# Performance work log

Measured on AMD Instinct MI355X. Metric: run time of the kernel, lower is better.

The kernel has to match this reference:

```python
import jax, jax.numpy as jnp
import numpy as np
from jax.ops import segment_sum, segment_max

N_NODES, SEQ, D, V = 2048, 64, 256, 32000
NH, DH = 8, 32      # transformer heads, head dim
GH = 4              # GAT heads (concat=False -> mean over heads)
E = 32768
NEG_INF = -1e9


def _pe(max_len, d):
    pos = np.arange(max_len)[:, None].astype(np.float32)
    div = np.exp(np.arange(0, d, 2).astype(np.float32) * (-np.log(10000.0) / d))
    pe = np.zeros((max_len, d), np.float32)
    pe[:, 0::2] = np.sin(pos * div)
    pe[:, 1::2] = np.cos(pos * div)
    return jnp.asarray(pe)


def _ln(x, g, b, eps=1e-5):
    m = x.mean(-1, keepdims=True)
    v = jnp.var(x, axis=-1, keepdims=True)
    return (x - m) / jnp.sqrt(v + eps) * g + b


def _encoder(x, Wqkv, bqkv, Wo, bo, ln1g, ln1b, ln2g, ln2b, W1, b1, W2, b2):
    # nn.TransformerEncoder, post-norm, relu, dropout off (eval)
    for l in range(2):
        qkv = x @ Wqkv[l] + bqkv[l]
        q, k, v = jnp.split(qkv, 3, -1)
        hds = lambda t: t.reshape(N_NODES, SEQ, NH, DH).transpose(0, 2, 1, 3)
        q, k, v = hds(q), hds(k), hds(v)
        att = jax.nn.softmax(jnp.einsum('bhqd,bhkd->bhqk', q, k) / np.sqrt(DH).astype(np.float32), -1)
        o = jnp.einsum('bhqk,bhkd->bhqd', att, v).transpose(0, 2, 1, 3).reshape(N_NODES, SEQ, D)
        x = _ln(x + o @ Wo[l] + bo[l], ln1g[l], ln1b[l])
        ff = jax.nn.relu(x @ W1[l] + b1[l]) @ W2[l] + b2[l]
        x = _ln(x + ff, ln2g[l], ln2b[l])
    return x


def _gat(xt, W, b, asrc, adst, src, dst, emask):
    # PyG GATConv(heads=4, concat=False): self-loops added, LeakyReLU(0.2),
    # softmax over incoming edges per destination, mean over heads, + bias.
    x = (xt @ W).reshape(N_NODES, GH, D)              # [N,GH,D]
    a_s = jnp.sum(x * asrc, -1)                        # [N,GH]
    a_d = jnp.sum(x * adst, -1)
    e = jax.nn.leaky_relu(a_s[src] + a_d[dst], 0.2)    # [E,GH]
    e = jnp.where(emask[:, None], e, NEG_INF)
    e_self = jax.nn.leaky_relu(a_s + a_d, 0.2)         # [N,GH] self loops
    m = jnp.maximum(segment_max(e, dst, num_segments=N_NODES), e_self)
    w = jnp.where(emask[:, None], jnp.exp(e - m[dst]), 0.0)
    w_self = jnp.exp(e_self - m)
    denom = segment_sum(w, dst, num_segments=N_NODES) + w_self
    num = segment_sum(w[:, :, None] * x[src], dst, num_segments=N_NODES) + w_self[:, :, None] * x
    return (num / denom[:, :, None]).mean(1) + b


def setup_inputs():
    key = jax.random.key(0)
    ks = iter(jax.random.split(key, 40))
    g = lambda shape, s=0.02: jax.random.normal(next(ks), shape, jnp.float32) * s
    return dict(
        tok_emb=g((V, D)),
        enc_Wqkv=g((2, D, 3 * D)), enc_bqkv=jnp.zeros((2, 3 * D)),
        enc_Wo=g((2, D, D)), enc_bo=jnp.zeros((2, D)),
        enc_ln1_g=jnp.ones((2, D)), enc_ln1_b=jnp.zeros((2, D)),
        enc_ln2_g=jnp.ones((2, D)), enc_ln2_b=jnp.zeros((2, D)),
        enc_W1=g((2, D, D)), enc_b1=jnp.zeros((2, D)),
        enc_W2=g((2, D, D)), enc_b2=jnp.zeros((2, D)),
        type_emb=g((10, D)),
        msg_W=g((3, D, D)), msg_b=jnp.zeros((3, D)),
        gat_W=g((4, D, GH * D)), gat_b=jnp.zeros((4, D)),
        gat_asrc=g((4, GH, D)), gat_adst=g((4, GH, D)),
        sp_W1=g((D, 512)), sp_b1=jnp.zeros((512,)),
        sp_W2=g((512, D)), sp_b2=jnp.zeros((D,)),
        log_c=jnp.zeros((1,)),
        rule_token_seqs=jax.random.randint(next(ks), (N_NODES, SEQ), 0, V),
        rule_types=jax.random.randint(next(ks), (N_NODES,), 0, 10),
        edge_index=jax.random.randint(next(ks), (2, E), 0, N_NODES),
        edge_type=jax.random.randint(next(ks), (E,), 0, 3),
    )


def reference(tok_emb, enc_Wqkv, enc_bqkv, enc_Wo, enc_bo, enc_ln1_g, enc_ln1_b,
              enc_ln2_g, enc_ln2_b, enc_W1, enc_b1, enc_W2, enc_b2, type_emb,
              msg_W, msg_b, gat_W, gat_b, gat_asrc, gat_adst,
              sp_W1, sp_b1, sp_W2, sp_b2, log_c,
              rule_token_seqs, rule_types, edge_index, edge_type):
    # logic encoder
    x = tok_emb[rule_token_seqs] * np.sqrt(D).astype(np.float32) + _pe(SEQ, D)[None]
    x = _encoder(x, enc_Wqkv, enc_bqkv, enc_Wo, enc_bo, enc_ln1_g, enc_ln1_b,
                 enc_ln2_g, enc_ln2_b, enc_W1, enc_b1, enc_W2, enc_b2)
    h = x.mean(1) + type_emb[rule_types]                 # node_features [N,D]
    # logical GNN: per-relation linear + GATConv, summed, residual, relu
    src, dst = edge_index[0], edge_index[1]
    for l in range(4):
        h_new = 0.0
        for r in range(3):
            th = h @ msg_W[r] + msg_b[r]
            h_new = h_new + _gat(th, gat_W[l], gat_b[l], gat_asrc[l], gat_adst[l],
                                 src, dst, edge_type == r)
        h = jax.nn.relu(h + h_new)
    pos = jax.nn.relu(h @ sp_W1 + sp_b1) @ sp_W2 + sp_b2
    tang = jnp.tanh(pos) * 2.0
    st = tang * jnp.sqrt(jnp.exp(log_c))                 # scaled tangent [N,D]
    # Lorentz exp_map0 of v = [0, st]: ||v||_L = ||st||
    r = jnp.maximum(jnp.linalg.norm(st, axis=-1, keepdims=True), 1e-8)
    return jnp.concatenate([jnp.cosh(r), jnp.sinh(r) / r * st], -1)  # [N, D+1]
```

## Files before the change

### kernel.cpp

```cpp
#include <hip/hip_runtime.h>
#include <hip/hip_bf16.h>

#define NN 2048
#define SEQL 64
#define DIM 256
#define NHEAD 8
#define EDGES 32768
#define CHUNKS 2
#define CN (NN / CHUNKS)
#define CROWS (CN * SEQL)

typedef __attribute__((ext_vector_type(8))) short short8;
typedef __attribute__((ext_vector_type(4))) float f32x4;
typedef __attribute__((ext_vector_type(4))) unsigned short us4;
typedef unsigned short ushort_t;

__device__ __forceinline__ float us2f(unsigned short u) {
    union { unsigned int i; float f; } x; x.i = ((unsigned int)u) << 16; return x.f;
}
__device__ __forceinline__ unsigned short f2us(float f) {
    union { float f; unsigned int i; } u; u.f = f;
    unsigned int r = u.i + 0x7fffu + ((u.i >> 16) & 1u);
    return (unsigned short)(r >> 16);
}
__device__ __forceinline__ float lrelu02(float v) { return v < 0.f ? 0.2f * v : v; }

__device__ __forceinline__ void gload_lds16(const void* g, void* l) {
    __builtin_amdgcn_global_load_lds(
        (const __attribute__((address_space(1))) unsigned int*)g,
        (__attribute__((address_space(3))) unsigned int*)l, 16, 0, 0);
}

__global__ void sniff_kernel(const unsigned int* __restrict__ w, int* __restrict__ flag) {
    __shared__ int cnt;
    if (threadIdx.x == 0) cnt = 0;
    __syncthreads();
    unsigned int v = w[(size_t)threadIdx.x * 509];
    unsigned int e_lo = (v >> 7) & 0xffu;
    if (e_lo >= 0x6eu && e_lo <= 0x7fu) atomicAdd(&cnt, 1);
    __syncthreads();
    if (threadIdx.x == 0) *flag = (cnt > 128) ? 1 : 0;
}

#define NE 33
struct ConvArgs {
    const void* src[NE];
    unsigned int soff[NE];
    unsigned int off[NE + 1];
    unsigned int nel[NE];
    unsigned short ncol[NE];
    unsigned char klog2[NE];
};

__global__ void convert_kernel(ConvArgs a, const int* __restrict__ flag,
                               ushort_t* __restrict__ dst, unsigned int total) {
    const int bf = *flag;
    for (unsigned int i = blockIdx.x * 256 + threadIdx.x; i < total; i += gridDim.x * 256) {
        int e = 0;
        while (a.off[e + 1] <= i) ++e;
        unsigned int j = i - a.off[e];
        ushort_t v = 0;
        if (j < a.nel[e]) {
            unsigned int sidx;
            if (a.klog2[e]) {
                unsigned int K = 1u << a.klog2[e];
                unsigned int k = j & (K - 1), n = j >> a.klog2[e];
                sidx = k * (unsigned int)a.ncol[e] + n;
            } else sidx = j;
            sidx += a.soff[e];
            if (bf) v = ((const ushort_t*)a.src[e])[sidx];
            else    v = f2us(((const float*)a.src[e])[sidx]);
        }
        dst[i] = v;
    }
}

template <int K, bool RELU, bool OUT_BF16>
__global__ __launch_bounds__(256) void gemm_bt(
    const ushort_t* __restrict__ A, const ushort_t* __restrict__ BT,
    const ushort_t* __restrict__ bias, void* __restrict__ C,
    int N, int lda, size_t a_off_z, size_t c_off_z)
{
    __shared__ __align__(16) short a_lds[2][128][32];
    __shared__ __align__(16) short b_lds[2][128][32];

    const int tid  = threadIdx.x;
    const int lane = tid & 63;
    const int wave = tid >> 6;
    const int wr = wave >> 1, wc = wave & 1;

    const int gx = gridDim.x, gy = gridDim.y;
    const int nwg = gx * gy;
    const int lin = blockIdx.y * gx + blockIdx.x;
    const int q8 = nwg >> 3;
    const int sid = (lin & 7) * q8 + (lin >> 3);
    const int mb = sid / gy;
    const int nb = sid - mb * gy;
    const size_t mbase = (size_t)mb * 128;
    const size_t nbase = (size_t)nb * 128;

    A += (size_t)blockIdx.z * a_off_z;
    const size_t czoff = (size_t)blockIdx.z * c_off_z;

    f32x4 acc[4][4];
    const f32x4 fzero = {0.f, 0.f, 0.f, 0.f};
#pragma unroll
    for (int i = 0; i < 4; ++i)
#pragma unroll
        for (int j = 0; j < 4; ++j) acc[i][j] = fzero;

    const int srow = tid >> 2;
    const int ksw0 = (((tid & 3) ^ ((srow >> 1) & 3)) * 8);
    const int rl = lane & 15;
    const int kfs = (((lane >> 4) ^ ((rl >> 1) & 3)) * 8);

    constexpr int nk = K >> 5;
    auto stage = [&](int buf, int k0) {
        short* lA = &a_lds[buf][0][0] + wave * 512;
        short* lB = &b_lds[buf][0][0] + wave * 512;
        gload_lds16(A  + (mbase + srow)      * (size_t)lda + k0 + ksw0, lA);
        gload_lds16(A  + (mbase + srow + 64) * (size_t)lda + k0 + ksw0, lA + 2048);
        gload_lds16(BT + (nbase + srow)      * (size_t)K   + k0 + ksw0, lB);
        gload_lds16(BT + (nbase + srow + 64) * (size_t)K   + k0 + ksw0, lB + 2048);
    };

    stage(0, 0);
    if (nk > 1) stage(1, 32);
#pragma unroll
    for (int t = 0; t < nk; ++t) {
        const int cur = t & 1;
        if (t + 1 < nk) { asm volatile("s_waitcnt vmcnt(4)" ::: "memory"); }
        else            { asm volatile("s_waitcnt vmcnt(0)" ::: "memory"); }
        __builtin_amdgcn_s_barrier();
        __builtin_amdgcn_sched_barrier(0);

        short8 af[4], bfr[4];
#pragma unroll
        for (int m = 0; m < 4; ++m) af[m]  = *(const short8*)&a_lds[cur][wr * 64 + m * 16 + rl][kfs];
#pragma unroll
        for (int n = 0; n < 4; ++n) bfr[n] = *(const short8*)&b_lds[cur][wc * 64 + n * 16 + rl][kfs];
        asm volatile("s_waitcnt lgkmcnt(0)" ::: "memory");
        __builtin_amdgcn_sched_barrier(0);
#pragma unroll
        for (int m = 0; m < 4; ++m)
#pragma unroll
            for (int n = 0; n < 4; ++n)
                acc[m][n] = __builtin_amdgcn_mfma_f32_16x16x32_bf16(af[m], bfr[n], acc[m][n], 0, 0, 0);
        __builtin_amdgcn_s_barrier();
        __builtin_amdgcn_sched_barrier(0);
        if (t + 2 < nk) stage(cur, (t + 2) * 32);
    }

    const int rq = (lane >> 4) * 4;
#pragma unroll
    for (int m = 0; m < 4; ++m) {
#pragma unroll
        for (int n = 0; n < 4; ++n) {
            size_t gcol = nbase + wc * 64 + n * 16 + rl;
            float bv = bias ? us2f(bias[gcol]) : 0.f;
#pragma unroll
            for (int p = 0; p < 4; ++p) {
                size_t grow = mbase + wr * 64 + m * 16 + rq + p;
                float v = acc[m][n][p] + bv;
                if (RELU) v = fmaxf(v, 0.f);
                if (OUT_BF16) ((ushort_t*)C)[czoff + grow * N + gcol] = f2us(v);
                else          ((float*)C)[czoff + grow * N + gcol] = v;
            }
        }
    }
}

template <int K>
__global__ __launch_bounds__(512) void gemm_ln(
    const ushort_t* __restrict__ A, const ushort_t* __restrict__ BT,
    const ushort_t* __restrict__ bias, ushort_t* __restrict__ X,
    const ushort_t* __restrict__ gg, const ushort_t* __restrict__ bb)
{
    __shared__ __align__(16) short a_lds[2][128][32];
    __shared__ __align__(16) short b_lds[2][256][32];
    __shared__ float st_part[128][8];
    __shared__ float st_fin[128][2];

    const int tid  = threadIdx.x;
    const int lane = tid & 63;
    const int wave = tid >> 6;
    const int wr = wave >> 2, wc = wave & 3;
    const size_t mbase = (size_t)blockIdx.x * 128;

    f32x4 acc[4][4];
    const f32x4 fzero = {0.f, 0.f, 0.f, 0.f};
#pragma unroll
    for (int i = 0; i < 4; ++i)
#pragma unroll
        for (int j = 0; j < 4; ++j) acc[i][j] = fzero;

    const int srow = tid >> 2;
    const int ksw0 = (((tid & 3) ^ ((srow >> 1) & 3)) * 8);
    const int rl = lane & 15;
    const int g  = lane >> 4;
    const int kfs = ((g ^ ((rl >> 1) & 3)) * 8);

    constexpr int nk = K >> 5;
    auto stage = [&](int buf, int k0) {
        gload_lds16(A  + (mbase + srow) * (size_t)K + k0 + ksw0,
                    &a_lds[buf][0][0] + wave * 512);
        gload_lds16(BT + (size_t)srow         * K + k0 + ksw0,
                    &b_lds[buf][0][0] + wave * 512);
        gload_lds16(BT + (size_t)(srow + 128) * K + k0 + ksw0,
                    &b_lds[buf][0][0] + wave * 512 + 4096);
    };

    stage(0, 0);
    if (nk > 1) stage(1, 32);
#pragma unroll
    for (int t = 0; t < nk; ++t) {
        const int cur = t & 1;
        if (t + 1 < nk) { asm volatile("s_waitcnt vmcnt(3)" ::: "memory"); }
        else            { asm volatile("s_waitcnt vmcnt(0)" ::: "memory"); }
        __builtin_amdgcn_s_barrier();
        __builtin_amdgcn_sched_barrier(0);

        short8 af[4], bfr[4];
#pragma unroll
        for (int m = 0; m < 4; ++m) af[m]  = *(const short8*)&a_lds[cur][wr * 64 + m * 16 + rl][kfs];
#pragma unroll
        for (int n = 0; n < 4; ++n) bfr[n] = *(const short8*)&b_lds[cur][wc * 64 + n * 16 + rl][kfs];
        asm volatile("s_waitcnt lgkmcnt(0)" ::: "memory");
        __builtin_amdgcn_sched_barrier(0);
#pragma unroll
        for (int m = 0; m < 4; ++m)
#pragma unroll
            for (int n = 0; n < 4; ++n)
                acc[m][n] = __builtin_amdgcn_mfma_f32_16x16x32_bf16(af[m], bfr[n], acc[m][n], 0, 0, 0);
        __builtin_amdgcn_s_barrier();
        __builtin_amdgcn_sched_barrier(0);
        if (t + 2 < nk) stage(cur, (t + 2) * 32);
    }

#pragma unroll
    for (int m = 0; m < 4; ++m)
#pragma unroll
        for (int n = 0; n < 4; ++n) {
            int gcol = wc * 64 + n * 16 + rl;
            float bv = us2f(bias[gcol]);
#pragma unroll
            for (int r = 0; r < 4; ++r) {
                size_t grow = mbase + wr * 64 + m * 16 + g * 4 + r;
                acc[m][n][r] += bv + us2f(X[grow * 256 + gcol]);
            }
        }
#pragma unroll
    for (int m = 0; m < 4; ++m)
#pragma unroll
        for (int r = 0; r < 4; ++r) {
            float ps = 0.f, pq = 0.f;
#pragma unroll
            for (int n = 0; n < 4; ++n) { float v = acc[m][n][r]; ps += v; pq += v * v; }
#pragma unroll
            for (int off = 1; off < 16; off <<= 1) { ps += __shfl_xor(ps, off); pq += __shfl_xor(pq, off); }
            if (rl == 0) {
                int row = wr * 64 + m * 16 + g * 4 + r;
                st_part[row][wc] = ps;
                st_part[row][4 + wc] = pq;
            }
        }
    __syncthreads();
    if (tid < 128) {
        float s = st_part[tid][0] + st_part[tid][1] + st_part[tid][2] + st_part[tid][3];
        float q = st_part[tid][4] + st_part[tid][5] + st_part[tid][6] + st_part[tid][7];
        float mean = s * (1.f / 256.f);
        float var = q * (1.f / 256.f) - mean * mean;
        st_fin[tid][0] = mean;
        st_fin[tid][1] = rsqrtf(var + 1e-5f);
    }
    __syncthreads();
#pragma unroll
    for (int m = 0; m < 4; ++m)
#pragma unroll
        for (int n = 0; n < 4; ++n) {
            int gcol = wc * 64 + n * 16 + rl;
            float gv = us2f(gg[gcol]), bv = us2f(bb[gcol]);
#pragma unroll
            for (int r = 0; r < 4; ++r) {
                int row = wr * 64 + m * 16 + g * 4 + r;
                float out = (acc[m][n][r] - st_fin[row][0]) * st_fin[row][1] * gv + bv;
                X[(mbase + row) * 256 + gcol] = f2us(out);
            }
        }
}

__global__ __launch_bounds__(128) void attn_mfma(const ushort_t* __restrict__ qkv,
                                                 ushort_t* __restrict__ O) {
    __shared__ ushort_t smem[2][6912];
    const int w = threadIdx.x >> 6, lane = threadIdx.x & 63;
    const int h = blockIdx.y * 2 + w;
    const int rl = lane & 15, g = lane >> 4;
    const size_t rowbase = (size_t)blockIdx.x * 64;
    ushort_t* vt = smem[w];
    ushort_t* pl = smem[w] + 2304;

    const ushort_t* vp = qkv + (rowbase + lane) * 768 + 512 + h * 32;
#pragma unroll
    for (int i = 0; i < 4; ++i) {
        union { short8 v; ushort_t s[8]; } u;
        u.v = *(const short8*)(vp + i * 8);
#pragma unroll
        for (int j = 0; j < 8; ++j) vt[(i * 8 + j) * 72 + lane] = u.s[j];
    }

    short8 kf[4], qf[4];
#pragma unroll
    for (int t = 0; t < 4; ++t) {
        kf[t] = *(const short8*)(qkv + (rowbase + t * 16 + rl) * 768 + 256 + h * 32 + g * 8);
        qf[t] = *(const short8*)(qkv + (rowbase + t * 16 + rl) * 768 +       h * 32 + g * 8);
    }

    f32x4 s[4][4];
    const f32x4 fzero = {0.f, 0.f, 0.f, 0.f};
#pragma unroll
    for (int kt = 0; kt < 4; ++kt)
#pragma unroll
        for (int qt = 0; qt < 4; ++qt) s[kt][qt] = fzero;
#pragma unroll
    for (int kt = 0; kt < 4; ++kt)
#pragma unroll
        for (int qt = 0; qt < 4; ++qt)
            s[kt][qt] = __builtin_amdgcn_mfma_f32_16x16x32_bf16(kf[kt], qf[qt], s[kt][qt], 0, 0, 0);

    const float sc = 0.17677669529663687f;
    float inv[4];
#pragma unroll
    for (int qt = 0; qt < 4; ++qt) {
        float m = -1e30f;
#pragma unroll
        for (int kt = 0; kt < 4; ++kt)
#pragma unroll
            for (int r = 0; r < 4; ++r) { s[kt][qt][r] *= sc; m = fmaxf(m, s[kt][qt][r]); }
        m = fmaxf(m, __shfl_xor(m, 16));
        m = fmaxf(m, __shfl_xor(m, 32));
        float sum = 0.f;
#pragma unroll
        for (int kt = 0; kt < 4; ++kt)
#pragma unroll
            for (int r = 0; r < 4; ++r) { float e = __expf(s[kt][qt][r] - m); s[kt][qt][r] = e; sum += e; }
        sum += __shfl_xor(sum, 16);
        sum += __shfl_xor(sum, 32);
        inv[qt] = 1.f / sum;
    }

#pragma unroll
    for (int qt = 0; qt < 4; ++qt)
#pragma unroll
        for (int kt = 0; kt < 4; ++kt) {
            us4 pk;
#pragma unroll
            for (int r = 0; r < 4; ++r) pk[r] = f2us(s[kt][qt][r] * inv[qt]);
            *(us4*)&pl[(qt * 16 + rl) * 72 + kt * 16 + g * 4] = pk;
        }
    asm volatile("s_waitcnt lgkmcnt(0)" ::: "memory");
    __builtin_amdgcn_sched_barrier(0);

    f32x4 o[2][4];
#pragma unroll
    for (int dt = 0; dt < 2; ++dt)
#pragma unroll
        for (int qt = 0; qt < 4; ++qt) o[dt][qt] = fzero;
#pragma unroll
    for (int ks = 0; ks < 2; ++ks) {
        short8 va[2];
#pragma unroll
        for (int dt = 0; dt < 2; ++dt)
            va[dt] = *(const short8*)&vt[(dt * 16 + rl) * 72 + ks * 32 + g * 8];
#pragma unroll
        for (int qt = 0; qt < 4; ++qt) {
            short8 pb = *(const short8*)&pl[(qt * 16 + rl) * 72 + ks * 32 + g * 8];
#pragma unroll
            for (int dt = 0; dt < 2; ++dt)
                o[dt][qt] = __builtin_amdgcn_mfma_f32_16x16x32_bf16(va[dt], pb, o[dt][qt], 0, 0, 0);
        }
    }

#pragma unroll
    for (int dt = 0; dt < 2; ++dt)
#pragma unroll
        for (int qt = 0; qt < 4; ++qt) {
            us4 ov;
#pragma unroll
            for (int r = 0; r < 4; ++r) ov[r] = f2us(o[dt][qt][r]);
            *(us4*)&pl[(qt * 16 + rl) * 40 + dt * 16 + g * 4] = ov;
        }
    asm volatile("s_waitcnt lgkmcnt(0)" ::: "memory");
    __builtin_amdgcn_sched_barrier(0);
    ushort_t* op = O + (rowbase + lane) * 256 + h * 32;
#pragma unroll
    for (int t = 0; t < 4; ++t)
        *(short8*)(op + t * 8) = *(const short8*)&pl[lane * 40 + t * 8];
}

__global__ void pe_kernel(float* __restrict__ pe) {
    int s = blockIdx.x, d = threadIdx.x;
    int i = d >> 1;
    float freq = __expf((float)(2 * i) * (-9.210340371976184f / 256.f));
    float ang = (float)s * freq;
    pe[s * DIM + d] = (d & 1) ? cosf(ang) : sinf(ang);
}

__global__ __launch_bounds__(64) void embed_kernel(const void* __restrict__ tok_emb,
                                                   const int* __restrict__ flag,
                                                   const int* __restrict__ tokens,
                                                   const float* __restrict__ pe,
                                                   ushort_t* __restrict__ X, int row0) {
    int lr = blockIdx.x, t = threadIdx.x;
    int grow = row0 + lr;
    int tok = tokens[grow];
    int s = grow & 63;
    int d0 = t * 4;
    size_t idx = (size_t)tok * DIM + d0;
    f32x4 pv = *(const f32x4*)&pe[s * DIM + d0];
    us4 out;
    if (*flag) {
        us4 tv = *(const us4*)((const ushort_t*)tok_emb + idx);
#pragma unroll
        for (int j = 0; j < 4; ++j) out[j] = f2us(us2f(tv[j]) * 16.f + pv[j]);
    } else {
        f32x4 tv = *(const f32x4*)((const float*)tok_emb + idx);
#pragma unroll
        for (int j = 0; j < 4; ++j) out[j] = f2us(tv[j] * 16.f + pv[j]);
    }
    *(us4*)&X[(size_t)lr * DIM + d0] = out;
}

__global__ void mean_kernel(const ushort_t* __restrict__ Xc,
                            const ushort_t* __restrict__ type_emb,
                            const int* __restrict__ rtypes,
                            float* __restrict__ h, ushort_t* __restrict__ hb, int n0) {
    int nl = blockIdx.x, d = threadIdx.x;
    float acc = 0.f;
    for (int s = 0; s < 64; ++s) acc += us2f(Xc[((size_t)nl * 64 + s) * DIM + d]);
    int n = n0 + nl;
    float val = acc * (1.f / 64.f) + us2f(type_emb[(size_t)rtypes[n] * DIM + d]);
    h[(size_t)n * DIM + d] = val;
    hb[(size_t)n * DIM + d] = f2us(val);
}

__global__ void hist_kernel(const int* __restrict__ ei, int* __restrict__ counts) {
    int e = blockIdx.x * 256 + threadIdx.x;
    if (e < EDGES) atomicAdd(&counts[ei[EDGES + e]], 1);
}
__global__ __launch_bounds__(256) void scan_kernel(const int* __restrict__ counts,
                                                   int* __restrict__ indptr,
                                                   int* __restrict__ cursor) {
    __shared__ int part[256];
    int t = threadIdx.x;
    int local[8]; int s = 0;
#pragma unroll
    for (int i = 0; i < 8; ++i) { local[i] = s; s += counts[t * 8 + i]; }
    part[t] = s;
    __syncthreads();
    for (int d = 1; d < 256; d <<= 1) {
        int val = (t >= d) ? part[t - d] : 0;
        __syncthreads();
        part[t] += val;
        __syncthreads();
    }
    int base = part[t] - s;
#pragma unroll
    for (int i = 0; i < 8; ++i) { int v = base + local[i]; indptr[t * 8 + i] = v; cursor[t * 8 + i] = v; }
    if (t == 255) indptr[NN] = part[255];
}
__global__ void scatter_kernel(const int* __restrict__ ei, const int* __restrict__ et,
                               int* __restrict__ cursor, int* __restrict__ col_src,
                               int* __restrict__ col_type) {
    int e = blockIdx.x * 256 + threadIdx.x;
    if (e < EDGES) {
        int d = ei[EDGES + e];
        int pp = atomicAdd(&cursor[d], 1);
        col_src[pp] = ei[e];
        col_type[pp] = et[e];
    }
}

__global__ __launch_bounds__(256) void asad_kernel(const float* __restrict__ xg,
                                                   const ushort_t* __restrict__ asrc,
                                                   const ushort_t* __restrict__ adst,
                                                   float* __restrict__ a_s, float* __restrict__ a_d,
                                                   int l) {
    int n = blockIdx.x, r = blockIdx.y, g = threadIdx.x >> 6, lane = threadIdx.x & 63;
    const float* xp = xg + ((size_t)r * NN + n) * 1024 + g * 256 + lane * 4;
    const ushort_t* sp = asrc + ((size_t)l * 4 + g) * 256 + lane * 4;
    const ushort_t* dp = adst + ((size_t)l * 4 + g) * 256 + lane * 4;
    float ss = 0.f, dd = 0.f;
#pragma unroll
    for (int j = 0; j < 4; ++j) { float x = xp[j]; ss += x * us2f(sp[j]); dd += x * us2f(dp[j]); }
#pragma unroll
    for (int off = 32; off > 0; off >>= 1) { ss += __shfl_xor(ss, off); dd += __shfl_xor(dd, off); }
    if (lane == 0) {
        a_s[((size_t)r * NN + n) * 4 + g] = ss;
        a_d[((size_t)r * NN + n) * 4 + g] = dd;
    }
}

__global__ __launch_bounds__(256) void edge_kernel(const float* __restrict__ xg,
                                                   const float* __restrict__ a_s,
                                                   const float* __restrict__ a_d,
                                                   const int* __restrict__ indptr,
                                                   const int* __restrict__ col_src,
                                                   const int* __restrict__ col_type,
                                                   const ushort_t* __restrict__ gat_b,
                                                   float* __restrict__ hnew3, int l) {
    __shared__ float outs[4][256];
    int n = blockIdx.x, r = blockIdx.y, g = threadIdx.x >> 6, lane = threadIdx.x & 63;
    int beg = indptr[n], end = indptr[n + 1];
    const size_t rb = (size_t)r * NN;
    float adn = a_d[(rb + n) * 4 + g];
    float eself = lrelu02(a_s[(rb + n) * 4 + g] + adn);
    float m = eself;
    for (int e = beg; e < end; ++e) {
        if (col_type[e] == r) {
            float v = lrelu02(a_s[(rb + col_src[e]) * 4 + g] + adn);
            m = fmaxf(m, v);
        }
    }
    float wself = __expf(eself - m);
    float denom = wself;
    const float* xn = xg + (rb + n) * 1024 + g * 256 + lane * 4;
    float num[4];
#pragma unroll
    for (int j = 0; j < 4; ++j) num[j] = wself * xn[j];
    for (int e = beg; e < end; ++e) {
        if (col_type[e] == r) {
            int src = col_src[e];
            float v = lrelu02(a_s[(rb + src) * 4 + g] + adn);
            float w = __expf(v - m);
            denom += w;
            const float* xs = xg + (rb + src) * 1024 + g * 256 + lane * 4;
#pragma unroll
            for (int j = 0; j < 4; ++j) num[j] += w * xs[j];
        }
    }
    float invd = 1.f / denom;
#pragma unroll
    for (int j = 0; j < 4; ++j) outs[g][lane * 4 + j] = num[j] * invd;
    __syncthreads();
    int d = threadIdx.x;
    float hv = 0.25f * (outs[0][d] + outs[1][d] + outs[2][d] + outs[3][d]) + us2f(gat_b[l * 256 + d]);
    hnew3[(rb + n) * 256 + d] = hv;
}

__global__ void update_h_kernel(float* __restrict__ h, const float* __restrict__ hnew3,
                                ushort_t* __restrict__ hb) {
    size_t i = (size_t)blockIdx.x * 256 + threadIdx.x;
    float v = fmaxf(h[i] + hnew3[i] + hnew3[(size_t)NN * 256 + i] + hnew3[(size_t)2 * NN * 256 + i], 0.f);
    h[i] = v;
    hb[i] = f2us(v);
}

__global__ __launch_bounds__(64) void final_kernel(const float* __restrict__ pos,
                                                   const ushort_t* __restrict__ log_c,
                                                   const int* __restrict__ flag,
                                                   void* __restrict__ out) {
    int n = blockIdx.x, lane = threadIdx.x;
    int bf = *flag;
    float scv = sqrtf(__expf(us2f(log_c[0])));
    f32x4 pv = *(const f32x4*)&pos[(size_t)n * 256 + lane * 4];
    float st[4]; float sq = 0.f;
#pragma unroll
    for (int j = 0; j < 4; ++j) { float t = tanhf(pv[j]) * 2.f * scv; st[j] = t; sq += t * t; }
#pragma unroll
    for (int off = 32; off > 0; off >>= 1) sq += __shfl_xor(sq, off);
    float rr = fmaxf(sqrtf(sq), 1e-8f);
    float sf = sinhf(rr) / rr;
    if (bf) {
        ushort_t* o = (ushort_t*)out;
        if (lane == 0) o[(size_t)n * 257] = f2us(coshf(rr));
#pragma unroll
        for (int j = 0; j < 4; ++j) o[(size_t)n * 257 + 1 + lane * 4 + j] = f2us(sf * st[j]);
    } else {
        float* o = (float*)out;
        if (lane == 0) o[(size_t)n * 257] = coshf(rr);
#pragma unroll
        for (int j = 0; j < 4; ++j) o[(size_t)n * 257 + 1 + lane * 4 + j] = sf * st[j];
    }
}

extern "C" void kernel_launch(void* const* d_in, const int* in_sizes, int n_in,
                              void* d_out, int out_size, void* d_ws, size_t ws_size,
                              hipStream_t stream) {
    const int* tokens = (const int*)d_in[25];
    const int* rtypes = (const int*)d_in[26];
    const int* eidx   = (const int*)d_in[27];
    const int* etype  = (const int*)d_in[28];

    char* base = (char*)d_ws;
    size_t pos = 0;
    auto alloc = [&](size_t b) -> char* {
        char* r = base + pos; pos = (pos + b + 255) & ~(size_t)255; return r;
    };

    int* flag = (int*)alloc(256);

    ConvArgs ca;
    int ne = 0; unsigned int off = 0;
    auto add = [&](const void* src, unsigned int soff, unsigned int elems,
                   int klog2, int ncol) -> unsigned int {
        ca.src[ne] = src; ca.soff[ne] = soff; ca.off[ne] = off;
        ca.nel[ne] = elems; ca.klog2[ne] = (unsigned char)klog2;
        ca.ncol[ne] = (unsigned short)ncol;
        unsigned int r = off; off += (elems + 7) & ~7u; ++ne; return r;
    };
    unsigned int oWqkv = add(d_in[1], 0, 196608, 8, 768);
                         add(d_in[1], 196608, 196608, 8, 768);
    unsigned int obqkv = add(d_in[2], 0, 1536, 0, 0);
    unsigned int oWo   = add(d_in[3], 0, 65536, 8, 256);
                         add(d_in[3], 65536, 65536, 8, 256);
    unsigned int obo   = add(d_in[4], 0, 512, 0, 0);
    unsigned int oln1g = add(d_in[5], 0, 512, 0, 0);
    unsigned int oln1b = add(d_in[6], 0, 512, 0, 0);
    unsigned int oln2g = add(d_in[7], 0, 512, 0, 0);
    unsigned int oln2b = add(d_in[8], 0, 512, 0, 0);
    unsigned int oW1   = add(d_in[9], 0, 65536, 8, 256);
                         add(d_in[9], 65536, 65536, 8, 256);
    unsigned int ob1   = add(d_in[10], 0, 512, 0, 0);
    unsigned int oW2   = add(d_in[11], 0, 65536, 8, 256);
                         add(d_in[11], 65536, 65536, 8, 256);
    unsigned int ob2   = add(d_in[12], 0, 512, 0, 0);
    unsigned int otype = add(d_in[13], 0, 2560, 0, 0);
    unsigned int omsgW = add(d_in[14], 0, 65536, 8, 256);
                         add(d_in[14], 65536, 65536, 8, 256);
                         add(d_in[14], 131072, 65536, 8, 256);
    unsigned int omsgb = add(d_in[15], 0, 768, 0, 0);
    unsigned int ogatW = add(d_in[16], 0, 262144, 8, 1024);
                         add(d_in[16], 262144, 262144, 8, 1024);
                         add(d_in[16], 524288, 262144, 8, 1024);
                         add(d_in[16], 786432, 262144, 8, 1024);
    unsigned int ogatb = add(d_in[17], 0, 1024, 0, 0);
    unsigned int oasrc = add(d_in[18], 0, 4096, 0, 0);
    unsigned int oadst = add(d_in[19], 0, 4096, 0, 0);
    unsigned int ospW1 = add(d_in[20], 0, 131072, 8, 512);
    unsigned int ospb1 = add(d_in[21], 0, 512, 0, 0);
    unsigned int ospW2 = add(d_in[22], 0, 131072, 9, 256);
    unsigned int ospb2 = add(d_in[23], 0, 256, 0, 0);
    unsigned int ologc = add(d_in[24], 0, 1, 0, 0);
    ca.off[ne] = off;
    unsigned int wtotal = off;

    ushort_t* wtb   = (ushort_t*)alloc((size_t)wtotal * 2);
    float*    pe    = (float*)   alloc((size_t)SEQL * DIM * 4);
    float*    h     = (float*)   alloc((size_t)NN * DIM * 4);
    ushort_t* hb    = (ushort_t*)alloc((size_t)NN * DIM * 2);
    float*    a_s   = (float*)   alloc((size_t)3 * NN * 4 * 4);
    float*    a_d   = (float*)   alloc((size_t)3 * NN * 4 * 4);
    int*      counts = (int*)    alloc((size_t)NN * 4);
    int*      indptr = (int*)    alloc((size_t)(NN + 1) * 4);
    int*      cursor = (int*)    alloc((size_t)NN * 4);
    int*      col_src  = (int*)  alloc((size_t)EDGES * 4);
    int*      col_type = (int*)  alloc((size_t)EDGES * 4);

    size_t spos0 = pos;
    ushort_t* Xc  = (ushort_t*)alloc((size_t)CROWS * DIM * 2);
    ushort_t* QKV = (ushort_t*)alloc((size_t)CROWS * 768 * 2);
    ushort_t* Oc  = (ushort_t*)alloc((size_t)CROWS * DIM * 2);
    pos = spos0;
    ushort_t* th    = (ushort_t*)alloc((size_t)NN * 768 * 2);
    float*    xg    = (float*)   alloc((size_t)3 * NN * 1024 * 4);
    float*    hnew3 = (float*)   alloc((size_t)3 * NN * DIM * 4);
    ushort_t* thead = (ushort_t*)alloc((size_t)NN * 512 * 2);
    float*    posb  = (float*)   alloc((size_t)NN * DIM * 4);

    const ushort_t* WqkvT = wtb + oWqkv;
    const ushort_t* bqkv  = wtb + obqkv;
    const ushort_t* WoT   = wtb + oWo;
    const ushort_t* bo    = wtb + obo;
    const ushort_t* ln1g  = wtb + oln1g;
    const ushort_t* ln1b  = wtb + oln1b;
    const ushort_t* ln2g  = wtb + oln2g;
    const ushort_t* ln2b  = wtb + oln2b;
    const ushort_t* W1T   = wtb + oW1;
    const ushort_t* b1    = wtb + ob1;
    const ushort_t* W2T   = wtb + oW2;
    const ushort_t* b2    = wtb + ob2;
    const ushort_t* type_emb = wtb + otype;
    const ushort_t* msgWT = wtb + omsgW;
    const ushort_t* msg_b = wtb + omsgb;
    const ushort_t* gatWT = wtb + ogatW;
    const ushort_t* gat_b = wtb + ogatb;
    const ushort_t* gasrc = wtb + oasrc;
    const ushort_t* gadst = wtb + oadst;
    const ushort_t* spW1T = wtb + ospW1;
    const ushort_t* spb1  = wtb + ospb1;
    const ushort_t* spW2T = wtb + ospW2;
    const ushort_t* spb2  = wtb + ospb2;
    const ushort_t* log_c = wtb + ologc;

    sniff_kernel<<<1, 256, 0, stream>>>((const unsigned int*)d_in[1], flag);
    convert_kernel<<<2048, 256, 0, stream>>>(ca, flag, wtb, wtotal);

    pe_kernel<<<SEQL, DIM, 0, stream>>>(pe);
    hipMemsetAsync(counts, 0, NN * 4, stream);
    hist_kernel<<<EDGES / 256, 256, 0, stream>>>(eidx, counts);
    scan_kernel<<<1, 256, 0, stream>>>(counts, indptr, cursor);
    scatter_kernel<<<EDGES / 256, 256, 0, stream>>>(eidx, etype, cursor, col_src, col_type);

    for (int c = 0; c < CHUNKS; ++c) {
        int row0 = c * CROWS;
        embed_kernel<<<CROWS, 64, 0, stream>>>(d_in[0], flag, tokens, pe, Xc, row0);
        for (int l = 0; l < 2; ++l) {
            gemm_bt<256, false, true><<<dim3(CROWS / 128, 6), 256, 0, stream>>>(
                Xc, WqkvT + (size_t)l * 196608, bqkv + l * 768, QKV, 768, DIM, 0, 0);
            attn_mfma<<<dim3(CN, 4), 128, 0, stream>>>(QKV, Oc);
            gemm_ln<256><<<CROWS / 128, 512, 0, stream>>>(
                Oc, WoT + (size_t)l * 65536, bo + l * DIM, Xc, ln1g + l * DIM, ln1b + l * DIM);
            gemm_bt<256, true, true><<<dim3(CROWS / 128, 2), 256, 0, stream>>>(
                Xc, W1T + (size_t)l * 65536, b1 + l * DIM, Oc, DIM, DIM, 0, 0);
            gemm_ln<256><<<CROWS / 128, 512, 0, stream>>>(
                Oc, W2T + (size_t)l * 65536, b2 + l * DIM, Xc, ln2g + l * DIM, ln2b + l * DIM);
        }
        mean_kernel<<<CN, DIM, 0, stream>>>(Xc, type_emb, rtypes, h, hb, c * CN);
    }

    for (int l = 0; l < 4; ++l) {
        gemm_bt<256, false, true><<<dim3(NN / 128, 6), 256, 0, stream>>>(
            hb, msgWT, msg_b, th, 768, DIM, 0, 0);
        gemm_bt<256, false, false><<<dim3(NN / 128, 8, 3), 256, 0, stream>>>(
            th, gatWT + (size_t)l * 262144, nullptr, xg, 1024, 768,
            (size_t)256, (size_t)NN * 1024);
        asad_kernel<<<dim3(NN, 3), 256, 0, stream>>>(xg, gasrc, gadst, a_s, a_d, l);
        edge_kernel<<<dim3(NN, 3), 256, 0, stream>>>(xg, a_s, a_d, indptr, col_src, col_type,
                                                     gat_b, hnew3, l);
        update_h_kernel<<<NN, 256, 0, stream>>>(h, hnew3, hb);
    }

    gemm_bt<256, true, true><<<dim3(NN / 128, 4), 256, 0, stream>>>(
        hb, spW1T, spb1, thead, 512, DIM, 0, 0);
    gemm_bt<512, false, false><<<dim3(NN / 128, 2), 256, 0, stream>>>(
        thead, spW2T, spb2, posb, DIM, 512, 0, 0);
    final_kernel<<<NN, 64, 0, stream>>>(posb, log_c, flag, d_out);
}
```

Measured before the change: 1.126 ms.

## Fuse FFN into one LN kernel, bf16 GAT features, LDS-staged GEMM epilogue

Adds an ffn_ln kernel that computes relu(X·W1+b1) into LDS and immediately multiplies by W2 with residual and LayerNorm, removing the intermediate FFN activation round trip and one launch per layer. Attention now writes its output in place into the QKV buffer, which gemm_ln reads through a new lda stride, so the separate O buffer goes away. The bf16 gemm_bt epilogue stages the tile through swizzled LDS so global stores are 16-byte vectors. The GAT projection output xg is stored as bf16 instead of fp32, halving gather traffic in the asad and edge kernels at some precision cost. Embedding and mean run once over all rows instead of per chunk.

```diff
diff --git a/kernel.cpp b/kernel.cpp
--- a/kernel.cpp
+++ b/kernel.cpp
@@ -6,9 +6,10 @@
 #define DIM 256
 #define NHEAD 8
 #define EDGES 32768
+#define CROWS (NN * SEQL)
 #define CHUNKS 2
 #define CN (NN / CHUNKS)
-#define CROWS (CN * SEQL)
+#define CRC (CROWS / CHUNKS)
 
 typedef __attribute__((ext_vector_type(8))) short short8;
 typedef __attribute__((ext_vector_type(4))) float f32x4;
@@ -81,8 +82,7 @@
     const ushort_t* __restrict__ bias, void* __restrict__ C,
     int N, int lda, size_t a_off_z, size_t c_off_z)
 {
-    __shared__ __align__(16) short a_lds[2][128][32];
-    __shared__ __align__(16) short b_lds[2][128][32];
+    __shared__ __align__(16) short smem[16384];
 
     const int tid  = threadIdx.x;
     const int lane = tid & 63;
@@ -116,8 +116,8 @@
 
     constexpr int nk = K >> 5;
     auto stage = [&](int buf, int k0) {
-        short* lA = &a_lds[buf][0][0] + wave * 512;
-        short* lB = &b_lds[buf][0][0] + wave * 512;
+        short* lA = smem + buf * 4096 + wave * 512;
+        short* lB = smem + 8192 + buf * 4096 + wave * 512;
         gload_lds16(A  + (mbase + srow)      * (size_t)lda + k0 + ksw0, lA);
         gload_lds16(A  + (mbase + srow + 64) * (size_t)lda + k0 + ksw0, lA + 2048);
         gload_lds16(BT + (nbase + srow)      * (size_t)K   + k0 + ksw0, lB);
@@ -136,9 +136,11 @@
 
         short8 af[4], bfr[4];
 #pragma unroll
-        for (int m = 0; m < 4; ++m) af[m]  = *(const short8*)&a_lds[cur][wr * 64 + m * 16 + rl][kfs];
-#pragma unroll
-        for (int n = 0; n < 4; ++n) bfr[n] = *(const short8*)&b_lds[cur][wc * 64 + n * 16 + rl][kfs];
+        for (int m = 0; m < 4; ++m)
+            af[m]  = *(const short8*)&smem[cur * 4096 + (wr * 64 + m * 16 + rl) * 32 + kfs];
+#pragma unroll
+        for (int n = 0; n < 4; ++n)
+            bfr[n] = *(const short8*)&smem[8192 + cur * 4096 + (wc * 64 + n * 16 + rl) * 32 + kfs];
         asm volatile("s_waitcnt lgkmcnt(0)" ::: "memory");
         __builtin_amdgcn_sched_barrier(0);
 #pragma unroll
@@ -152,27 +154,54 @@
     }
 
     const int rq = (lane >> 4) * 4;
-#pragma unroll
-    for (int m = 0; m < 4; ++m) {
-#pragma unroll
-        for (int n = 0; n < 4; ++n) {
-            size_t gcol = nbase + wc * 64 + n * 16 + rl;
-            float bv = bias ? us2f(bias[gcol]) : 0.f;
-#pragma unroll
-            for (int p = 0; p < 4; ++p) {
-                size_t grow = mbase + wr * 64 + m * 16 + rq + p;
-                float v = acc[m][n][p] + bv;
-                if (RELU) v = fmaxf(v, 0.f);
-                if (OUT_BF16) ((ushort_t*)C)[czoff + grow * N + gcol] = f2us(v);
-                else          ((float*)C)[czoff + grow * N + gcol] = v;
+    if (OUT_BF16) {
+#pragma unroll
+        for (int m = 0; m < 4; ++m)
+#pragma unroll
+            for (int n = 0; n < 4; ++n) {
+                int lcol = wc * 64 + n * 16 + rl;
+                float bv = bias ? us2f(bias[nbase + lcol]) : 0.f;
+                int chunk = lcol >> 3;
+#pragma unroll
+                for (int q = 0; q < 4; ++q) {
+                    int row = wr * 64 + m * 16 + rq + q;
+                    float v = acc[m][n][q] + bv;
+                    if (RELU) v = fmaxf(v, 0.f);
+                    smem[row * 128 + (((chunk ^ (row & 7)) << 3) | (lcol & 7))] = (short)f2us(v);
+                }
             }
-        }
+        asm volatile("s_waitcnt lgkmcnt(0)" ::: "memory");
+        __builtin_amdgcn_s_barrier();
+        __builtin_amdgcn_sched_barrier(0);
+#pragma unroll
+        for (int j = 0; j < 8; ++j) {
+            int hw = tid * 8 + j * 2048;
+            int row = hw >> 7;
+            int ch  = tid & 15;
+            short8 v = *(const short8*)&smem[row * 128 + ((ch ^ (row & 7)) << 3)];
+            *(short8*)((ushort_t*)C + czoff + (mbase + row) * (size_t)N + nbase + ch * 8) = v;
+        }
+    } else {
+#pragma unroll
+        for (int m = 0; m < 4; ++m)
+#pragma unroll
+            for (int n = 0; n < 4; ++n) {
+                size_t gcol = nbase + wc * 64 + n * 16 + rl;
+                float bv = bias ? us2f(bias[gcol]) : 0.f;
+#pragma unroll
+                for (int q = 0; q < 4; ++q) {
+                    size_t grow = mbase + wr * 64 + m * 16 + rq + q;
+                    float v = acc[m][n][q] + bv;
+                    if (RELU) v = fmaxf(v, 0.f);
+                    ((float*)C)[czoff + grow * N + gcol] = v;
+                }
+            }
     }
 }
 
 template <int K>
 __global__ __launch_bounds__(512) void gemm_ln(
-    const ushort_t* __restrict__ A, const ushort_t* __restrict__ BT,
+    const ushort_t* __restrict__ A, int lda, const ushort_t* __restrict__ BT,
     const ushort_t* __restrict__ bias, ushort_t* __restrict__ X,
     const ushort_t* __restrict__ gg, const ushort_t* __restrict__ bb)
 {
@@ -202,7 +231,7 @@
 
     constexpr int nk = K >> 5;
     auto stage = [&](int buf, int k0) {
-        gload_lds16(A  + (mbase + srow) * (size_t)K + k0 + ksw0,
+        gload_lds16(A  + (mbase + srow) * (size_t)lda + k0 + ksw0,
                     &a_lds[buf][0][0] + wave * 512);
         gload_lds16(BT + (size_t)srow         * K + k0 + ksw0,
                     &b_lds[buf][0][0] + wave * 512);
@@ -289,8 +318,181 @@
         }
 }
 
-__global__ __launch_bounds__(128) void attn_mfma(const ushort_t* __restrict__ qkv,
-                                                 ushort_t* __restrict__ O) {
+__global__ __launch_bounds__(256) void ffn_ln(
+    ushort_t* __restrict__ X,
+    const ushort_t* __restrict__ W1T, const ushort_t* __restrict__ b1,
+    const ushort_t* __restrict__ W2T, const ushort_t* __restrict__ b2,
+    const ushort_t* __restrict__ gg, const ushort_t* __restrict__ bb)
+{
+    __shared__ __align__(16) short a_lds[2][64][32];
+    __shared__ __align__(16) short b_lds[2][256][32];
+    __shared__ __align__(16) short T[64 * 256];
+    __shared__ float st_part[64][8];
+    __shared__ float st_fin[64][2];
+
+    const int tid  = threadIdx.x;
+    const int lane = tid & 63;
+    const int wc   = tid >> 6;
+    const size_t mbase = (size_t)blockIdx.x * 64;
+    const int rl = lane & 15;
+    const int g  = lane >> 4;
+    const int kfs = ((g ^ ((rl >> 1) & 3)) * 8);
+
+    const int arow = tid >> 2;
+    const int ksw0 = (((tid & 3) ^ ((arow >> 1) & 3)) * 8);
+
+    f32x4 acc[4][4];
+    const f32x4 fzero = {0.f, 0.f, 0.f, 0.f};
+#pragma unroll
+    for (int i = 0; i < 4; ++i)
+#pragma unroll
+        for (int j = 0; j < 4; ++j) acc[i][j] = fzero;
+
+    auto stage1 = [&](int buf, int k0) {
+        gload_lds16(X + (mbase + arow) * (size_t)256 + k0 + ksw0,
+                    &a_lds[buf][0][0] + wc * 512);
+#pragma unroll
+        for (int p = 0; p < 4; ++p)
+            gload_lds16(W1T + (size_t)(arow + p * 64) * 256 + k0 + ksw0,
+                        &b_lds[buf][0][0] + p * 2048 + wc * 512);
+    };
+    auto stage2 = [&](int buf, int k0) {
+#pragma unroll
+        for (int p = 0; p < 4; ++p)
+            gload_lds16(W2T + (size_t)(arow + p * 64) * 256 + k0 + ksw0,
+                        &b_lds[buf][0][0] + p * 2048 + wc * 512);
+    };
+
+    stage1(0, 0);
+    stage1(1, 32);
+#pragma unroll
+    for (int t = 0; t < 8; ++t) {
+        const int cur = t & 1;
+        if (t + 1 < 8) { asm volatile("s_waitcnt vmcnt(5)" ::: "memory"); }
+        else           { asm volatile("s_waitcnt vmcnt(0)" ::: "memory"); }
+        __builtin_amdgcn_s_barrier();
+        __builtin_amdgcn_sched_barrier(0);
+
+        short8 af[4], bfr[4];
+#pragma unroll
+        for (int m = 0; m < 4; ++m) af[m]  = *(const short8*)&a_lds[cur][m * 16 + rl][kfs];
+#pragma unroll
+        for (int n = 0; n < 4; ++n) bfr[n] = *(const short8*)&b_lds[cur][wc * 64 + n * 16 + rl][kfs];
+        asm volatile("s_waitcnt lgkmcnt(0)" ::: "memory");
+        __builtin_amdgcn_sched_barrier(0);
+#pragma unroll
+        for (int m = 0; m < 4; ++m)
+#pragma unroll
+            for (int n = 0; n < 4; ++n)
+                acc[m][n] = __builtin_amdgcn_mfma_f32_16x16x32_bf16(af[m], bfr[n], acc[m][n], 0, 0, 0);
+        __builtin_amdgcn_s_barrier();
+        __builtin_amdgcn_sched_barrier(0);
+        if (t + 2 < 8) stage1(cur, (t + 2) * 32);
+    }
+
+    stage2(0, 0);
+    stage2(1, 32);
+
+#pragma unroll
+    for (int m = 0; m < 4; ++m)
+#pragma unroll
+        for (int n = 0; n < 4; ++n) {
+            int lcol = wc * 64 + n * 16 + rl;
+            float bv = us2f(b1[lcol]);
+            int chunk = lcol >> 3;
+#pragma unroll
+            for (int q = 0; q < 4; ++q) {
+                int row = m * 16 + g * 4 + q;
+                float v = fmaxf(acc[m][n][q] + bv, 0.f);
+                T[row * 256 + (((chunk ^ (row & 7)) << 3) | (lcol & 7))] = (short)f2us(v);
+            }
+            acc[m][n] = fzero;
+        }
+    asm volatile("s_waitcnt lgkmcnt(0)" ::: "memory");
+    __builtin_amdgcn_s_barrier();
+    __builtin_amdgcn_sched_barrier(0);
+
+#pragma unroll
+    for (int t = 0; t < 8; ++t) {
+        const int cur = t & 1;
+        if (t + 1 < 8) { asm volatile("s_waitcnt vmcnt(4)" ::: "memory"); }
+        else           { asm volatile("s_waitcnt vmcnt(0)" ::: "memory"); }
+        __builtin_amdgcn_s_barrier();
+        __builtin_amdgcn_sched_barrier(0);
+
+        short8 af[4], bfr[4];
+#pragma unroll
+        for (int m = 0; m < 4; ++m) {
+            int row = m * 16 + rl;
+            af[m] = *(const short8*)&T[row * 256 + (((t * 4 + g) ^ (row & 7)) << 3)];
+        }
+#pragma unroll
+        for (int n = 0; n < 4; ++n) bfr[n] = *(const short8*)&b_lds[cur][wc * 64 + n * 16 + rl][kfs];
+        asm volatile("s_waitcnt lgkmcnt(0)" ::: "memory");
+        __builtin_amdgcn_sched_barrier(0);
+#pragma unroll
+        for (int m = 0; m < 4; ++m)
+#pragma unroll
+            for (int n = 0; n < 4; ++n)
+                acc[m][n] = __builtin_amdgcn_mfma_f32_16x16x32_bf16(af[m], bfr[n], acc[m][n], 0, 0, 0);
+        __builtin_amdgcn_s_barrier();
+        __builtin_amdgcn_sched_barrier(0);
+        if (t + 2 < 8) stage2(cur, (t + 2) * 32);
+    }
+
+#pragma unroll
+    for (int m = 0; m < 4; ++m)
+#pragma unroll
+        for (int n = 0; n < 4; ++n) {
+            int gcol = wc * 64 + n * 16 + rl;
+            float bv = us2f(b2[gcol]);
+#pragma unroll
+            for (int r = 0; r < 4; ++r) {
+                size_t grow = mbase + m * 16 + g * 4 + r;
+                acc[m][n][r] += bv + us2f(X[grow * 256 + gcol]);
+            }
+        }
+#pragma unroll
+    for (int m = 0; m < 4; ++m)
+#pragma unroll
+        for (int r = 0; r < 4; ++r) {
+            float ps = 0.f, pq = 0.f;
+#pragma unroll
+            for (int n = 0; n < 4; ++n) { float v = acc[m][n][r]; ps += v; pq += v * v; }
+#pragma unroll
+            for (int off = 1; off < 16; off <<= 1) { ps += __shfl_xor(ps, off); pq += __shfl_xor(pq, off); }
+            if (rl == 0) {
+                int row = m * 16 + g * 4 + r;
+                st_part[row][wc] = ps;
+                st_part[row][4 + wc] = pq;
+            }
+        }
+    __syncthreads();
+    if (tid < 64) {
+        float s = st_part[tid][0] + st_part[tid][1] + st_part[tid][2] + st_part[tid][3];
+        float q = st_part[tid][4] + st_part[tid][5] + st_part[tid][6] + st_part[tid][7];
+        float mean = s * (1.f / 256.f);
+        float var = q * (1.f / 256.f) - mean * mean;
+        st_fin[tid][0] = mean;
+        st_fin[tid][1] = rsqrtf(var + 1e-5f);
+    }
+    __syncthreads();
+#pragma unroll
+    for (int m = 0; m < 4; ++m)
+#pragma unroll
+        for (int n = 0; n < 4; ++n) {
+            int gcol = wc * 64 + n * 16 + rl;
+            float gv = us2f(gg[gcol]), bv = us2f(bb[gcol]);
+#pragma unroll
+            for (int r = 0; r < 4; ++r) {
+                int row = m * 16 + g * 4 + r;
+                float out = (acc[m][n][r] - st_fin[row][0]) * st_fin[row][1] * gv + bv;
+                X[(mbase + row) * 256 + gcol] = f2us(out);
+            }
+        }
+}
+
+__global__ __launch_bounds__(128) void attn_mfma(ushort_t* __restrict__ qkv) {
     __shared__ ushort_t smem[2][6912];
     const int w = threadIdx.x >> 6, lane = threadIdx.x & 63;
     const int h = blockIdx.y * 2 + w;
@@ -391,7 +593,7 @@
         }
     asm volatile("s_waitcnt lgkmcnt(0)" ::: "memory");
     __builtin_amdgcn_sched_barrier(0);
-    ushort_t* op = O + (rowbase + lane) * 256 + h * 32;
+    ushort_t* op = qkv + (rowbase + lane) * 768 + h * 32;
 #pragma unroll
     for (int t = 0; t < 4; ++t)
         *(short8*)(op + t * 8) = *(const short8*)&pl[lane * 40 + t * 8];
@@ -405,13 +607,13 @@
     pe[s * DIM + d] = (d & 1) ? cosf(ang) : sinf(ang);
 }
 
-__global__ __launch_bounds__(64) void embed_kernel(const void* __restrict__ tok_emb,
-                                                   const int* __restrict__ flag,
-                                                   const int* __restrict__ tokens,
-                                                   const float* __restrict__ pe,
-                                                   ushort_t* __restrict__ X, int row0) {
-    int lr = blockIdx.x, t = threadIdx.x;
-    int grow = row0 + lr;
+__global__ __launch_bounds__(256) void embed_kernel(const void* __restrict__ tok_emb,
+                                                    const int* __restrict__ flag,
+                                                    const int* __restrict__ tokens,
+                                                    const float* __restrict__ pe,
+                                                    ushort_t* __restrict__ X) {
+    int grow = blockIdx.x * 4 + (threadIdx.x >> 6);
+    int t = threadIdx.x & 63;
     int tok = tokens[grow];
     int s = grow & 63;
     int d0 = t * 4;
@@ -427,17 +629,16 @@
 #pragma unroll
         for (int j = 0; j < 4; ++j) out[j] = f2us(tv[j] * 16.f + pv[j]);
     }
-    *(us4*)&X[(size_t)lr * DIM + d0] = out;
+    *(us4*)&X[(size_t)grow * DIM + d0] = out;
 }
 
 __global__ void mean_kernel(const ushort_t* __restrict__ Xc,
                             const ushort_t* __restrict__ type_emb,
                             const int* __restrict__ rtypes,
-                            float* __restrict__ h, ushort_t* __restrict__ hb, int n0) {
-    int nl = blockIdx.x, d = threadIdx.x;
+                            float* __restrict__ h, ushort_t* __restrict__ hb) {
+    int n = blockIdx.x, d = threadIdx.x;
     float acc = 0.f;
-    for (int s = 0; s < 64; ++s) acc += us2f(Xc[((size_t)nl * 64 + s) * DIM + d]);
-    int n = n0 + nl;
+    for (int s = 0; s < 64; ++s) acc += us2f(Xc[((size_t)n * 64 + s) * DIM + d]);
     float val = acc * (1.f / 64.f) + us2f(type_emb[(size_t)rtypes[n] * DIM + d]);
     h[(size_t)n * DIM + d] = val;
     hb[(size_t)n * DIM + d] = f2us(val);
@@ -480,18 +681,19 @@
     }
 }
 
-__global__ __launch_bounds__(256) void asad_kernel(const float* __restrict__ xg,
+__global__ __launch_bounds__(256) void asad_kernel(const ushort_t* __restrict__ xg,
                                                    const ushort_t* __restrict__ asrc,
                                                    const ushort_t* __restrict__ adst,
                                                    float* __restrict__ a_s, float* __restrict__ a_d,
                                                    int l) {
     int n = blockIdx.x, r = blockIdx.y, g = threadIdx.x >> 6, lane = threadIdx.x & 63;
-    const float* xp = xg + ((size_t)r * NN + n) * 1024 + g * 256 + lane * 4;
+    const ushort_t* xp = xg + ((size_t)r * NN + n) * 1024 + g * 256 + lane * 4;
     const ushort_t* sp = asrc + ((size_t)l * 4 + g) * 256 + lane * 4;
     const ushort_t* dp = adst + ((size_t)l * 4 + g) * 256 + lane * 4;
+    us4 xv = *(const us4*)xp;
     float ss = 0.f, dd = 0.f;
 #pragma unroll
-    for (int j = 0; j < 4; ++j) { float x = xp[j]; ss += x * us2f(sp[j]); dd += x * us2f(dp[j]); }
+    for (int j = 0; j < 4; ++j) { float x = us2f(xv[j]); ss += x * us2f(sp[j]); dd += x * us2f(dp[j]); }
 #pragma unroll
     for (int off = 32; off > 0; off >>= 1) { ss += __shfl_xor(ss, off); dd += __shfl_xor(dd, off); }
     if (lane == 0) {
@@ -500,7 +702,7 @@
     }
 }
 
-__global__ __launch_bounds__(256) void edge_kernel(const float* __restrict__ xg,
+__global__ __launch_bounds__(256) void edge_kernel(const ushort_t* __restrict__ xg,
                                                    const float* __restrict__ a_s,
                                                    const float* __restrict__ a_d,
                                                    const int* __restrict__ indptr,
@@ -523,19 +725,19 @@
     }
     float wself = __expf(eself - m);
     float denom = wself;
-    const float* xn = xg + (rb + n) * 1024 + g * 256 + lane * 4;
+    us4 xn = *(const us4*)(xg + (rb + n) * 1024 + g * 256 + lane * 4);
     float num[4];
 #pragma unroll
-    for (int j = 0; j < 4; ++j) num[j] = wself * xn[j];
+    for (int j = 0; j < 4; ++j) num[j] = wself * us2f(xn[j]);
     for (int e = beg; e < end; ++e) {
         if (col_type[e] == r) {
             int src = col_src[e];
             float v = lrelu02(a_s[(rb + src) * 4 + g] + adn);
             float w = __expf(v - m);
             denom += w;
-            const float* xs = xg + (rb + src) * 1024 + g * 256 + lane * 4;
-#pragma unroll
-            for (int j = 0; j < 4; ++j) num[j] += w * xs[j];
+            us4 xs = *(const us4*)(xg + (rb + src) * 1024 + g * 256 + lane * 4);
+#pragma unroll
+            for (int j = 0; j < 4; ++j) num[j] += w * us2f(xs[j]);
         }
     }
     float invd = 1.f / denom;
@@ -656,13 +858,12 @@
     int*      col_src  = (int*)  alloc((size_t)EDGES * 4);
     int*      col_type = (int*)  alloc((size_t)EDGES * 4);
 
+    ushort_t* Xc  = (ushort_t*)alloc((size_t)CROWS * DIM * 2);
     size_t spos0 = pos;
-    ushort_t* Xc  = (ushort_t*)alloc((size_t)CROWS * DIM * 2);
-    ushort_t* QKV = (ushort_t*)alloc((size_t)CROWS * 768 * 2);
-    ushort_t* Oc  = (ushort_t*)alloc((size_t)CROWS * DIM * 2);
+    ushort_t* QKV = (ushort_t*)alloc((size_t)CRC * 768 * 2);
     pos = spos0;
     ushort_t* th    = (ushort_t*)alloc((size_t)NN * 768 * 2);
-    float*    xg    = (float*)   alloc((size_t)3 * NN * 1024 * 4);
+    ushort_t* xg    = (ushort_t*)alloc((size_t)3 * NN * 1024 * 2);
     float*    hnew3 = (float*)   alloc((size_t)3 * NN * DIM * 4);
     ushort_t* thead = (ushort_t*)alloc((size_t)NN * 512 * 2);
     float*    posb  = (float*)   alloc((size_t)NN * DIM * 4);
@@ -701,27 +902,26 @@
     scan_kernel<<<1, 256, 0, stream>>>(counts, indptr, cursor);
     scatter_kernel<<<EDGES / 256, 256, 0, stream>>>(eidx, etype, cursor, col_src, col_type);
 
+    embed_kernel<<<CROWS / 4, 256, 0, stream>>>(d_in[0], flag, tokens, pe, Xc);
     for (int c = 0; c < CHUNKS; ++c) {
-        int row0 = c * CROWS;
-        embed_kernel<<<CROWS, 64, 0, stream>>>(d_in[0], flag, tokens, pe, Xc, row0);
+        ushort_t* Xcc = Xc + (size_t)c * CRC * DIM;
         for (int l = 0; l < 2; ++l) {
-            gemm_bt<256, false, true><<<dim3(CROWS / 128, 6), 256, 0, stream>>>(
-                Xc, WqkvT + (size_t)l * 196608, bqkv + l * 768, QKV, 768, DIM, 0, 0);
-            attn_mfma<<<dim3(CN, 4), 128, 0, stream>>>(QKV, Oc);
-            gemm_ln<256><<<CROWS / 128, 512, 0, stream>>>(
-                Oc, WoT + (size_t)l * 65536, bo + l * DIM, Xc, ln1g + l * DIM, ln1b + l * DIM);
-            gemm_bt<256, true, true><<<dim3(CROWS / 128, 2), 256, 0, stream>>>(
-                Xc, W1T + (size_t)l * 65536, b1 + l * DIM, Oc, DIM, DIM, 0, 0);
-            gemm_ln<256><<<CROWS / 128, 512, 0, stream>>>(
-                Oc, W2T + (size_t)l * 65536, b2 + l * DIM, Xc, ln2g + l * DIM, ln2b + l * DIM);
-        }
-        mean_kernel<<<CN, DIM, 0, stream>>>(Xc, type_emb, rtypes, h, hb, c * CN);
-    }
+            gemm_bt<256, false, true><<<dim3(CRC / 128, 6), 256, 0, stream>>>(
+                Xcc, WqkvT + (size_t)l * 196608, bqkv + l * 768, QKV, 768, DIM, 0, 0);
+            attn_mfma<<<dim3(CN, 4), 128, 0, stream>>>(QKV);
+            gemm_ln<256><<<CRC / 128, 512, 0, stream>>>(
+                QKV, 768, WoT + (size_t)l * 65536, bo + l * DIM, Xcc, ln1g + l * DIM, ln1b + l * DIM);
+            ffn_ln<<<CRC / 64, 256, 0, stream>>>(
+                Xcc, W1T + (size_t)l * 65536, b1 + l * DIM, W2T + (size_t)l * 65536, b2 + l * DIM,
+                ln2g + l * DIM, ln2b + l * DIM);
+        }
+    }
+    mean_kernel<<<NN, DIM, 0, stream>>>(Xc, type_emb, rtypes, h, hb);
 
     for (int l = 0; l < 4; ++l) {
         gemm_bt<256, false, true><<<dim3(NN / 128, 6), 256, 0, stream>>>(
             hb, msgWT, msg_b, th, 768, DIM, 0, 0);
-        gemm_bt<256, false, false><<<dim3(NN / 128, 8, 3), 256, 0, stream>>>(
+        gemm_bt<256, false, true><<<dim3(NN / 128, 8, 3), 256, 0, stream>>>(
             th, gatWT + (size_t)l * 262144, nullptr, xg, 1024, 768,
             (size_t)256, (size_t)NN * 1024);
         asad_kernel<<<dim3(NN, 3), 256, 0, stream>>>(xg, gasrc, gadst, a_s, a_d, l);
```

Result: no change. 1.133 ms (+0.6%).
